# Kernel optimization log

Hardware: AMD Instinct MI355X
Metric: run time of the kernel (lower is better)

The kernel has to match this reference:

```python
import jax, jax.numpy as jnp
import numpy as np

B, P, K, F, H = 128, 200, 60, 4, 64   # events, points/event, knn k, feat dim, hidden
N = B * P


def setup_inputs() -> dict:
    key = jax.random.key(0)
    k0, k1, k2, k3 = jax.random.split(key, 4)
    x = jax.random.normal(k0, (N, F), jnp.float32)
    pos = jax.random.normal(k1, (N, 3), jnp.float32)
    batch = jnp.arange(N, dtype=jnp.int32) // P  # sorted event ids, equal-size events
    W1 = jax.random.normal(k2, (F + 3, H), jnp.float32) / np.sqrt(F + 3)
    b1 = jnp.zeros((H,), jnp.float32)
    W2 = jax.random.normal(k3, (H, H), jnp.float32) / np.sqrt(H)
    b2 = jnp.zeros((H,), jnp.float32)
    return {"x": x, "pos": pos, "batch": batch, "W1": W1, "b1": b1, "W2": W2, "b2": b2}


def _knn_edges(pos):
    """knn_graph(pos, K, batch, loop=False, flow='source_to_target').
    Equal-size events -> batched [B,P,P] pairwise distances, no cross-event edges."""
    p = pos.reshape(B, P, 3)
    d2 = jnp.sum((p[:, :, None, :] - p[:, None, :, :]) ** 2, axis=-1)  # [B,P,P]
    d2 = d2 + jnp.eye(P, dtype=d2.dtype) * 1e10                        # exclude self (loop=False)
    _, nbr = jax.lax.top_k(-d2, K)                                     # [B,P,K] local neighbor ids
    src = (nbr + (jnp.arange(B, dtype=nbr.dtype) * P)[:, None, None]).reshape(-1)  # sources j
    dst = jnp.repeat(jnp.arange(N, dtype=src.dtype), K)                             # targets i
    return jnp.stack([src, dst])  # [2, N*K]


def _local_nn(m, W1, b1, W2, b2):
    h = jax.nn.relu(m @ W1 + b1)
    return jax.nn.relu(h @ W2 + b2)


def reference(x, pos, batch, W1, b1, W2, b2):
    edge_index = _knn_edges(pos)
    src, dst = edge_index[0], edge_index[1]
    # PointConv message: net(concat[x_j, pos_j - pos_i]) on each edge
    rel = pos[src] - pos[dst]                             # [E,3]
    m = jnp.concatenate([x[src], rel], axis=-1)           # [E,F+3]
    h = _local_nn(m, W1, b1, W2, b2)                      # [E,H]
    out = h.reshape(N, K, H).max(axis=1)                  # max-aggregate per target node
    # PyG PointConv adds self-loops by default: message with rel = 0
    m_self = jnp.concatenate([x, jnp.zeros((N, 3), x.dtype)], axis=-1)
    h_self = _local_nn(m_self, W1, b1, W2, b2)            # [N,H]
    out = jnp.maximum(out, h_self)
    return (out, pos, batch, edge_index)
```

## Files before the change

### kernel.cpp

```cpp
#include <hip/hip_runtime.h>
#include <hip/hip_bf16.h>

typedef unsigned short ushort_t;
typedef unsigned int u32;
typedef unsigned long long u64;
typedef __attribute__((ext_vector_type(8))) short bf16x8;
typedef __attribute__((ext_vector_type(4))) float f32x4;
typedef __attribute__((ext_vector_type(4))) u32 u32x4;

#define NB 128
#define PP 200
#define KK 60
#define NN (NB*PP)
#define HH 64

#define OUT_OFF   0
#define POS_OFF   (NN*HH)
#define BATCH_OFF (POS_OFF + NN*3)
#define ESRC_OFF  (BATCH_OFF + NN)
#define EDST_OFF  (ESRC_OFF + NN*KK)

static __device__ __forceinline__ u32 packtr(float a, float b) {
    return __builtin_amdgcn_perm(__float_as_uint(b), __float_as_uint(a), 0x07060302u);
}
static __device__ __forceinline__ u32 prefix_lt(u64 b) {
    return __builtin_amdgcn_mbcnt_hi((u32)(b >> 32),
                                     __builtin_amdgcn_mbcnt_lo((u32)b, 0));
}

__global__ __launch_bounds__(256) void fused_kernel(const float* __restrict__ x,
                                                    const float* __restrict__ pos,
                                                    const float* __restrict__ W1,
                                                    const float* __restrict__ b1p,
                                                    const float* __restrict__ W2,
                                                    const float* __restrict__ b2p,
                                                    float* __restrict__ out) {
    __shared__ alignas(16) float xs[PP * 4];
    __shared__ alignas(16) float psl[PP * 3];
    __shared__ alignas(16) u32 jslot[4 * 128];
    __shared__ alignas(16) u32 msg[4 * 256];
    __shared__ alignas(16) u32 af[4 * 256];
    __shared__ alignas(16) u32 zrow[4];

    int tid = threadIdx.x, blk = blockIdx.x;
    int e = blk / 25;
    int pl0b = (blk % 25) * 8;
    int i0b  = e * PP + pl0b;

    if (tid < 200) ((f32x4*)xs)[tid]  = ((const f32x4*)x)[e * PP + tid];
    if (tid < 150) ((f32x4*)psl)[tid] = ((const f32x4*)pos)[e * 150 + tid];
    if (tid < 4)   zrow[tid] = 0u;
    __syncthreads();

    if (tid < 24) out[POS_OFF + i0b * 3 + tid] = psl[pl0b * 3 + tid];
    if (tid < 8)  out[BATCH_OFF + i0b + tid] = (float)e;

    int lane = tid & 63, wv = tid >> 6;
    int lo16 = lane & 15, hi16 = lane >> 4;
    int plA = pl0b + wv * 2, plB = plA + 1;
    int iA = e * PP + plA,   iB = iA + 1;

    float axA = psl[plA*3], ayA = psl[plA*3+1], azA = psl[plA*3+2];
    float axB = psl[plB*3], ayB = psl[plB*3+1], azB = psl[plB*3+2];

    u32 keyA[4], keyB[4];
    #pragma unroll
    for (int q = 0; q < 4; ++q) {
        int j = lane + q * 64;
        int jc = (j < PP) ? j : 0;
        float px = psl[jc*3], py = psl[jc*3+1], pz = psl[jc*3+2];
        float dxA = px-axA, dyA = py-ayA, dzA = pz-azA;
        float dxB = px-axB, dyB = py-ayB, dzB = pz-azB;
        float d2A = dxA*dxA + dyA*dyA + dzA*dzA;
        float d2B = dxB*dxB + dyB*dyB + dzB*dzB;
        keyA[q] = (j < PP && j != plA)
                ? ((__float_as_uint(d2A) & 0xFFFFFF00u) | (u32)j) : 0xFFFFFFFFu;
        keyB[q] = (j < PP && j != plB)
                ? ((__float_as_uint(d2B) & 0xFFFFFF00u) | (u32)j) : 0xFFFFFFFFu;
    }

    u32 loA = 0u, hiA = 0x7F800000u, loB = 0u, hiB = 0x7F800000u;
    int doneA = 0, doneB = 0;
    for (int it = 0; it < 32; ++it) {
        u32 mA = loA + ((hiA - loA) >> 1);
        u32 mB = loB + ((hiB - loB) >> 1);
        int cA = __builtin_popcountll(__ballot(keyA[0] < mA))
               + __builtin_popcountll(__ballot(keyA[1] < mA))
               + __builtin_popcountll(__ballot(keyA[2] < mA))
               + __builtin_popcountll(__ballot(keyA[3] < mA));
        int cB = __builtin_popcountll(__ballot(keyB[0] < mB))
               + __builtin_popcountll(__ballot(keyB[1] < mB))
               + __builtin_popcountll(__ballot(keyB[2] < mB))
               + __builtin_popcountll(__ballot(keyB[3] < mB));
        if (!doneA) {
            if (cA >= KK) hiA = mA; else loA = mA;
            doneA = (cA == KK) | (hiA - loA <= 1u);
        }
        if (!doneB) {
            if (cB >= KK) hiB = mB; else loB = mB;
            doneB = (cB == KK) | (hiB - loB <= 1u);
        }
        if (doneA & doneB) break;
    }

    const int jsb = wv * 128;
    if (lane >= KK) {
        jslot[jsb + lane]      = (u32)plA;
        jslot[jsb + 64 + lane] = (u32)plB;
    }
    #pragma unroll
    for (int t = 0; t < 2; ++t) {
        const u32* key = t ? keyB : keyA;
        u32 hh = t ? hiB : hiA;
        int i  = t ? iB : iA;
        u64 m0 = __ballot(key[0] < hh);
        u64 m1 = __ballot(key[1] < hh);
        u64 m2 = __ballot(key[2] < hh);
        u64 m3 = __ballot(key[3] < hh);
        u32 s1 = (u32)__builtin_popcountll(m0);
        u32 s2 = s1 + (u32)__builtin_popcountll(m1);
        u32 s3 = s2 + (u32)__builtin_popcountll(m2);
        u32 sl[4] = { prefix_lt(m0), s1 + prefix_lt(m1),
                      s2 + prefix_lt(m2), s3 + prefix_lt(m3) };
        #pragma unroll
        for (int q = 0; q < 4; ++q) {
            if (key[q] < hh) {
                u32 j = key[q] & 0xFFu;
                out[ESRC_OFF + i * KK + (int)sl[q]] = (float)(e * PP + (int)j);
                jslot[jsb + t * 64 + (int)sl[q]] = j;
            }
        }
        if (lane < KK) out[EDST_OFF + i * KK + lane] = (float)i;
    }

    bf16x8 w1f[4];
    #pragma unroll
    for (int th = 0; th < 4; ++th) {
        union { u32 w[4]; bf16x8 v; } u; u.w[0]=u.w[1]=u.w[2]=u.w[3]=0u;
        if (hi16 == 0) {
            int m = th * 16 + lo16;
            u.w[0] = packtr(W1[0*64+m], W1[1*64+m]);
            u.w[1] = packtr(W1[2*64+m], W1[3*64+m]);
            u.w[2] = packtr(W1[4*64+m], W1[5*64+m]);
            u.w[3] = packtr(W1[6*64+m], b1p[m]);
        }
        w1f[th] = u.v;
    }
    bf16x8 bfr[4][2];
    #pragma unroll
    for (int t = 0; t < 4; ++t)
        #pragma unroll
        for (int s = 0; s < 2; ++s) {
            union { u32 w[4]; bf16x8 v; } u;
            int col = t * 16 + lo16, kb = s * 32 + hi16 * 8;
            #pragma unroll
            for (int d = 0; d < 4; ++d)
                u.w[d] = packtr(W2[(kb + 2*d) * 64 + col], W2[(kb + 2*d + 1) * 64 + col]);
            bfr[t][s] = u.v;
        }
    float b2v[4];
    #pragma unroll
    for (int t = 0; t < 4; ++t) b2v[t] = b2p[t * 16 + lo16];

    const int msb = wv * 256;
    const int afb = wv * 256;
    for (int tl = 0; tl < 2; ++tl) {
        int i = iA + tl, pl = plA + tl;
        int jloc = (int)jslot[jsb + tl * 64 + lane];
        f32x4 xv = ((const f32x4*)xs)[jloc];
        float rx = psl[jloc*3]   - psl[pl*3];
        float ry = psl[jloc*3+1] - psl[pl*3+1];
        float rz = psl[jloc*3+2] - psl[pl*3+2];
        u32x4 mrow;
        mrow[0] = packtr(xv[0], xv[1]);
        mrow[1] = packtr(xv[2], xv[3]);
        mrow[2] = packtr(rx, ry);
        mrow[3] = packtr(rz, 1.0f);
        *(u32x4*)&msg[msb + lane * 4] = mrow;

        float rmax[4] = {-3.0e38f, -3.0e38f, -3.0e38f, -3.0e38f};
        #pragma unroll
        for (int rt = 0; rt < 4; ++rt) {
            const u32* mp = (hi16 == 0) ? &msg[msb + (rt * 16 + lo16) * 4] : zrow;
            union { u32 w[4]; bf16x8 v; } mu;
            *(u32x4*)mu.w = *(const u32x4*)mp;

            f32x4 c1[4];
            #pragma unroll
            for (int th = 0; th < 4; ++th)
                c1[th] = __builtin_amdgcn_mfma_f32_16x16x32_bf16(w1f[th], mu.v,
                                                                 (f32x4)0.f, 0, 0, 0);
            f32x4 acc[4];
            #pragma unroll
            for (int t = 0; t < 4; ++t) acc[t] = (f32x4)0.f;

            #pragma unroll
            for (int s = 0; s < 2; ++s) {
                #pragma unroll
                for (int thh = 0; thh < 2; ++thh) {
                    int th = s * 2 + thh;
                    u32 pk0 = packtr(fmaxf(c1[th][0], 0.f), fmaxf(c1[th][1], 0.f));
                    u32 pk1 = packtr(fmaxf(c1[th][2], 0.f), fmaxf(c1[th][3], 0.f));
                    int dlane = lo16 + ((thh * 2 + (hi16 >> 1)) << 4);
                    int dbase = (hi16 & 1) * 2;
                    af[afb + (dbase + 0) * 64 + dlane] = pk0;
                    af[afb + (dbase + 1) * 64 + dlane] = pk1;
                }
                union { u32 w[4]; bf16x8 v; } u;
                #pragma unroll
                for (int d = 0; d < 4; ++d)
                    u.w[d] = af[afb + d * 64 + lane];
                #pragma unroll
                for (int t = 0; t < 4; ++t)
                    acc[t] = __builtin_amdgcn_mfma_f32_16x16x32_bf16(u.v, bfr[t][s],
                                                                     acc[t], 0, 0, 0);
            }
            #pragma unroll
            for (int t = 0; t < 4; ++t) {
                rmax[t] = fmaxf(fmaxf(acc[t][0], acc[t][1]), rmax[t]);
                rmax[t] = fmaxf(fmaxf(acc[t][2], acc[t][3]), rmax[t]);
            }
        }
        #pragma unroll
        for (int t = 0; t < 4; ++t) {
            rmax[t] = fmaxf(rmax[t], __shfl_xor(rmax[t], 16, 64));
            rmax[t] = fmaxf(rmax[t], __shfl_xor(rmax[t], 32, 64));
        }
        if (lane < 16) {
            #pragma unroll
            for (int t = 0; t < 4; ++t)
                out[OUT_OFF + i * 64 + t * 16 + lane] = fmaxf(rmax[t] + b2v[t], 0.f);
        }
    }
}

extern "C" void kernel_launch(void* const* d_in, const int* in_sizes, int n_in,
                              void* d_out, int out_size, void* d_ws, size_t ws_size,
                              hipStream_t stream) {
    const float* x     = (const float*)d_in[0];
    const float* pos   = (const float*)d_in[1];
    const float* W1    = (const float*)d_in[3];
    const float* b1    = (const float*)d_in[4];
    const float* W2    = (const float*)d_in[5];
    const float* b2    = (const float*)d_in[6];
    float* out = (float*)d_out;
    (void)d_ws; (void)ws_size; (void)in_sizes; (void)n_in; (void)out_size;

    fused_kernel<<<dim3(NN / 8), dim3(256), 0, stream>>>(x, pos, W1, b1, W2, b2, out);
}
```

Before: 108.8 us.

## Stage packed weights in LDS, use permlane swaps, coalesce edge and output stores

W1/b1 and W2 are now converted to bf16 pairs once per block, cooperatively into shared memory. This replaces the per-lane strided global gathers and packing for the MFMA fragments. The layer-1-to-layer-2 fragment shuffle now uses permlane32/permlane16 swaps instead of an LDS round-trip. The bisection loop only evaluates ballots for unfinished queries, edge-index writes go out as coalesced per-lane stores after the slot scatter, and the final output is written by all 64 lanes at once. The cost is extra LDS and a larger prologue per block.

```diff
diff --git a/kernel.cpp b/kernel.cpp
--- a/kernel.cpp
+++ b/kernel.cpp
@@ -1,7 +1,6 @@
 #include <hip/hip_runtime.h>
 #include <hip/hip_bf16.h>
 
-typedef unsigned short ushort_t;
 typedef unsigned int u32;
 typedef unsigned long long u64;
 typedef __attribute__((ext_vector_type(8))) short bf16x8;
@@ -39,7 +38,9 @@
     __shared__ alignas(16) float psl[PP * 3];
     __shared__ alignas(16) u32 jslot[4 * 128];
     __shared__ alignas(16) u32 msg[4 * 256];
-    __shared__ alignas(16) u32 af[4 * 256];
+    __shared__ alignas(16) u32 pkW1[64 * 4];
+    __shared__ alignas(16) u32 pkW2T[64 * 33];
+    __shared__ alignas(16) float b2s[64];
     __shared__ alignas(16) u32 zrow[4];
 
     int tid = threadIdx.x, blk = blockIdx.x;
@@ -50,6 +51,19 @@
     if (tid < 200) ((f32x4*)xs)[tid]  = ((const f32x4*)x)[e * PP + tid];
     if (tid < 150) ((f32x4*)psl)[tid] = ((const f32x4*)pos)[e * 150 + tid];
     if (tid < 4)   zrow[tid] = 0u;
+
+    {
+        int m = tid & 63, d = tid >> 6;
+        float hiv = (d < 3) ? W1[(2*d + 1)*64 + m] : b1p[m];
+        pkW1[m*4 + d] = packtr(W1[(2*d)*64 + m], hiv);
+    }
+    #pragma unroll
+    for (int r = 0; r < 8; ++r) {
+        int idx = r * 256 + tid;
+        int kp = idx >> 6, col = idx & 63;
+        pkW2T[col*33 + kp] = packtr(W2[(2*kp)*64 + col], W2[(2*kp + 1)*64 + col]);
+    }
+    if (tid < 64) b2s[tid] = b2p[tid];
     __syncthreads();
 
     if (tid < 24) out[POS_OFF + i0b * 3 + tid] = psl[pl0b * 3 + tid];
@@ -81,22 +95,23 @@
 
     u32 loA = 0u, hiA = 0x7F800000u, loB = 0u, hiB = 0x7F800000u;
     int doneA = 0, doneB = 0;
-    for (int it = 0; it < 32; ++it) {
-        u32 mA = loA + ((hiA - loA) >> 1);
-        u32 mB = loB + ((hiB - loB) >> 1);
-        int cA = __builtin_popcountll(__ballot(keyA[0] < mA))
-               + __builtin_popcountll(__ballot(keyA[1] < mA))
-               + __builtin_popcountll(__ballot(keyA[2] < mA))
-               + __builtin_popcountll(__ballot(keyA[3] < mA));
-        int cB = __builtin_popcountll(__ballot(keyB[0] < mB))
-               + __builtin_popcountll(__ballot(keyB[1] < mB))
-               + __builtin_popcountll(__ballot(keyB[2] < mB))
-               + __builtin_popcountll(__ballot(keyB[3] < mB));
+    #pragma unroll 1
+    for (int it = 0; it < 40; ++it) {
         if (!doneA) {
+            u32 mA = loA + ((hiA - loA) >> 1);
+            int cA = __builtin_popcountll(__ballot(keyA[0] < mA))
+                   + __builtin_popcountll(__ballot(keyA[1] < mA))
+                   + __builtin_popcountll(__ballot(keyA[2] < mA))
+                   + __builtin_popcountll(__ballot(keyA[3] < mA));
             if (cA >= KK) hiA = mA; else loA = mA;
             doneA = (cA == KK) | (hiA - loA <= 1u);
         }
         if (!doneB) {
+            u32 mB = loB + ((hiB - loB) >> 1);
+            int cB = __builtin_popcountll(__ballot(keyB[0] < mB))
+                   + __builtin_popcountll(__ballot(keyB[1] < mB))
+                   + __builtin_popcountll(__ballot(keyB[2] < mB))
+                   + __builtin_popcountll(__ballot(keyB[3] < mB));
             if (cB >= KK) hiB = mB; else loB = mB;
             doneB = (cB == KK) | (hiB - loB <= 1u);
         }
@@ -112,7 +127,6 @@
     for (int t = 0; t < 2; ++t) {
         const u32* key = t ? keyB : keyA;
         u32 hh = t ? hiB : hiA;
-        int i  = t ? iB : iA;
         u64 m0 = __ballot(key[0] < hh);
         u64 m1 = __ballot(key[1] < hh);
         u64 m2 = __ballot(key[2] < hh);
@@ -123,27 +137,22 @@
         u32 sl[4] = { prefix_lt(m0), s1 + prefix_lt(m1),
                       s2 + prefix_lt(m2), s3 + prefix_lt(m3) };
         #pragma unroll
-        for (int q = 0; q < 4; ++q) {
-            if (key[q] < hh) {
-                u32 j = key[q] & 0xFFu;
-                out[ESRC_OFF + i * KK + (int)sl[q]] = (float)(e * PP + (int)j);
-                jslot[jsb + t * 64 + (int)sl[q]] = j;
-            }
-        }
-        if (lane < KK) out[EDST_OFF + i * KK + lane] = (float)i;
+        for (int q = 0; q < 4; ++q)
+            if (key[q] < hh) jslot[jsb + t * 64 + (int)sl[q]] = key[q] & 0xFFu;
+    }
+    if (lane < KK) {
+        out[ESRC_OFF + iA * KK + lane] = (float)(e * PP + (int)jslot[jsb + lane]);
+        out[ESRC_OFF + iB * KK + lane] = (float)(e * PP + (int)jslot[jsb + 64 + lane]);
+        out[EDST_OFF + iA * KK + lane] = (float)iA;
+        out[EDST_OFF + iB * KK + lane] = (float)iB;
     }
 
     bf16x8 w1f[4];
     #pragma unroll
     for (int th = 0; th < 4; ++th) {
-        union { u32 w[4]; bf16x8 v; } u; u.w[0]=u.w[1]=u.w[2]=u.w[3]=0u;
-        if (hi16 == 0) {
-            int m = th * 16 + lo16;
-            u.w[0] = packtr(W1[0*64+m], W1[1*64+m]);
-            u.w[1] = packtr(W1[2*64+m], W1[3*64+m]);
-            u.w[2] = packtr(W1[4*64+m], W1[5*64+m]);
-            u.w[3] = packtr(W1[6*64+m], b1p[m]);
-        }
+        union { u32 w[4]; bf16x8 v; } u;
+        if (hi16 == 0) *(u32x4*)u.w = *(const u32x4*)&pkW1[(th * 16 + lo16) * 4];
+        else { u.w[0] = u.w[1] = u.w[2] = u.w[3] = 0u; }
         w1f[th] = u.v;
     }
     bf16x8 bfr[4][2];
@@ -152,18 +161,17 @@
         #pragma unroll
         for (int s = 0; s < 2; ++s) {
             union { u32 w[4]; bf16x8 v; } u;
-            int col = t * 16 + lo16, kb = s * 32 + hi16 * 8;
-            #pragma unroll
-            for (int d = 0; d < 4; ++d)
-                u.w[d] = packtr(W2[(kb + 2*d) * 64 + col], W2[(kb + 2*d + 1) * 64 + col]);
+            int base = (t * 16 + lo16) * 33 + s * 16 + hi16 * 4;
+            #pragma unroll
+            for (int d = 0; d < 4; ++d) u.w[d] = pkW2T[base + d];
             bfr[t][s] = u.v;
         }
-    float b2v[4];
-    #pragma unroll
-    for (int t = 0; t < 4; ++t) b2v[t] = b2p[t * 16 + lo16];
+    float b2me = b2s[lane];
 
     const int msb = wv * 256;
-    const int afb = wv * 256;
+    const u32* mbase = (hi16 == 0) ? &msg[msb + lo16 * 4] : zrow;
+    const int mstep  = (hi16 == 0) ? 64 : 0;
+
     for (int tl = 0; tl < 2; ++tl) {
         int i = iA + tl, pl = plA + tl;
         int jloc = (int)jslot[jsb + tl * 64 + lane];
@@ -181,9 +189,8 @@
         float rmax[4] = {-3.0e38f, -3.0e38f, -3.0e38f, -3.0e38f};
         #pragma unroll
         for (int rt = 0; rt < 4; ++rt) {
-            const u32* mp = (hi16 == 0) ? &msg[msb + (rt * 16 + lo16) * 4] : zrow;
             union { u32 w[4]; bf16x8 v; } mu;
-            *(u32x4*)mu.w = *(const u32x4*)mp;
+            *(u32x4*)mu.w = *(const u32x4*)(mbase + rt * mstep);
 
             f32x4 c1[4];
             #pragma unroll
@@ -196,20 +203,21 @@
 
             #pragma unroll
             for (int s = 0; s < 2; ++s) {
-                #pragma unroll
-                for (int thh = 0; thh < 2; ++thh) {
-                    int th = s * 2 + thh;
-                    u32 pk0 = packtr(fmaxf(c1[th][0], 0.f), fmaxf(c1[th][1], 0.f));
-                    u32 pk1 = packtr(fmaxf(c1[th][2], 0.f), fmaxf(c1[th][3], 0.f));
-                    int dlane = lo16 + ((thh * 2 + (hi16 >> 1)) << 4);
-                    int dbase = (hi16 & 1) * 2;
-                    af[afb + (dbase + 0) * 64 + dlane] = pk0;
-                    af[afb + (dbase + 1) * 64 + dlane] = pk1;
+                u32 pe0 = packtr(fmaxf(c1[2*s][0], 0.f), fmaxf(c1[2*s][1], 0.f));
+                u32 pe1 = packtr(fmaxf(c1[2*s][2], 0.f), fmaxf(c1[2*s][3], 0.f));
+                u32 po0 = packtr(fmaxf(c1[2*s+1][0], 0.f), fmaxf(c1[2*s+1][1], 0.f));
+                u32 po1 = packtr(fmaxf(c1[2*s+1][2], 0.f), fmaxf(c1[2*s+1][3], 0.f));
+                union { u32 w[4]; bf16x8 v; } u;
+                {
+                    auto t0 = __builtin_amdgcn_permlane32_swap(pe0, po0, false, false);
+                    auto w0 = __builtin_amdgcn_permlane16_swap(t0[0], t0[1], false, false);
+                    u.w[0] = w0[0]; u.w[2] = w0[1];
                 }
-                union { u32 w[4]; bf16x8 v; } u;
-                #pragma unroll
-                for (int d = 0; d < 4; ++d)
-                    u.w[d] = af[afb + d * 64 + lane];
+                {
+                    auto t1 = __builtin_amdgcn_permlane32_swap(pe1, po1, false, false);
+                    auto w1 = __builtin_amdgcn_permlane16_swap(t1[0], t1[1], false, false);
+                    u.w[1] = w1[0]; u.w[3] = w1[1];
+                }
                 #pragma unroll
                 for (int t = 0; t < 4; ++t)
                     acc[t] = __builtin_amdgcn_mfma_f32_16x16x32_bf16(u.v, bfr[t][s],
@@ -226,11 +234,11 @@
             rmax[t] = fmaxf(rmax[t], __shfl_xor(rmax[t], 16, 64));
             rmax[t] = fmaxf(rmax[t], __shfl_xor(rmax[t], 32, 64));
         }
-        if (lane < 16) {
-            #pragma unroll
-            for (int t = 0; t < 4; ++t)
-                out[OUT_OFF + i * 64 + t * 16 + lane] = fmaxf(rmax[t] + b2v[t], 0.f);
-        }
+        float sel = rmax[0];
+        sel = (hi16 == 1) ? rmax[1] : sel;
+        sel = (hi16 == 2) ? rmax[2] : sel;
+        sel = (hi16 == 3) ? rmax[3] : sel;
+        out[OUT_OFF + i * 64 + lane] = fmaxf(sel + b2me, 0.f);
     }
 }
 
```

After: 110.2 us. Within noise of the previous version (+1.3%).
